# Kernel optimization log

Hardware: AMD Instinct MI355X
Metric: run time of the kernel (lower is better)

Reference implementation:

```python
import jax, jax.numpy as jnp
import numpy as np

# NF4 codebook (bitsandbytes nf4 data type, 16 levels)
NF4_TABLE = np.array([
    -1.0, -0.6961928009986877, -0.5250730514526367, -0.39491748809814453,
    -0.28444138169288635, -0.18477343022823334, -0.09105003625154495, 0.0,
    0.07958029955625534, 0.16093020141124725, 0.24611230194568634,
    0.33791524171829224, 0.44070982933044434, 0.5626170039176941,
    0.7229568362236023, 1.0], dtype=np.float32)

BLOCKSIZE = 64
SCALING = 32.0 / 16.0  # lora_alpha / r


def setup_inputs() -> dict:
    key = jax.random.key(0)
    k1, k2, k3, k4, k5 = jax.random.split(key, 5)
    tokens, in_f, out_f, r = 256, 4096, 11008, 16
    x = jax.random.normal(k1, (tokens, in_f), dtype=jnp.float32)
    q_codes = jax.random.randint(k2, (out_f, in_f), 0, 16, dtype=jnp.int32)
    absmax = jax.random.uniform(k3, (out_f, in_f // BLOCKSIZE), dtype=jnp.float32)
    lora_A = jax.random.normal(k4, (r, in_f), dtype=jnp.float32) * (1.0 / np.sqrt(in_f))
    lora_B = jax.random.normal(k5, (out_f, r), dtype=jnp.float32) * 0.02
    return {"x": x, "q_codes": q_codes, "absmax": absmax,
            "lora_A": lora_A, "lora_B": lora_B}


def reference(x, q_codes, absmax, lora_A, lora_B):
    out_f, in_f = q_codes.shape
    nf4 = jnp.asarray(NF4_TABLE, dtype=x.dtype)
    # Dequantize: codebook lookup, then per-block absmax scale.
    W = nf4[q_codes].reshape(out_f, in_f // BLOCKSIZE, BLOCKSIZE)
    W = (W * absmax[:, :, None]).reshape(out_f, in_f)  # [out_f, in_f]
    # Base 4-bit linear (no bias in bnb Linear4bit default here).
    base = x @ W.T  # [tokens, out_f]
    # LoRA path: dropout p=0 is identity in eval; scaling = alpha/r.
    lora = (x @ lora_A.T) @ lora_B.T  # [tokens, r] -> [tokens, out_f]
    return base + lora * jnp.asarray(SCALING, dtype=x.dtype)
```

## Files before the change

### kernel.cpp

```cpp
#include <hip/hip_runtime.h>
#include <hip/hip_fp16.h>

typedef unsigned int uint;
typedef unsigned short ushort;

typedef __attribute__((ext_vector_type(8))) _Float16 f16x8;
typedef __attribute__((ext_vector_type(4))) float f32x4;

#define TOK 256
#define OUTF 11008
#define INF 4096
#define BM 256
#define BN 64
#define NT2 172

__device__ __constant__ float NF4_TBL[16] = {
    -1.0f, -0.6961928009986877f, -0.5250730514526367f, -0.39491748809814453f,
    -0.28444138169288635f, -0.18477343022823334f, -0.09105003625154495f, 0.0f,
    0.07958029955625534f, 0.16093020141124725f, 0.24611230194568634f,
    0.33791524171829224f, 0.44070982933044434f, 0.5626170039176941f,
    0.7229568362236023f, 1.0f};

__device__ __forceinline__ ushort f2h(float f) {
  return __half_as_ushort(__float2half(f));
}

__device__ __forceinline__ void async_cp16(const void* g, void* l) {
  __builtin_amdgcn_global_load_lds(
      (const __attribute__((address_space(1))) uint*)g,
      (__attribute__((address_space(3))) uint*)l, 16, 0, 0);
}

__global__ void prep_kernel(const int4* __restrict__ qc4, uint* __restrict__ pk,
                            const float4* __restrict__ x4, ushort4* __restrict__ xh4,
                            const float4* __restrict__ lB4, ushort4* __restrict__ lBh4) {
  const int stride = gridDim.x * blockDim.x;
  const int t0 = blockIdx.x * blockDim.x + threadIdx.x;
  for (int d = t0; d < OUTF * INF / 8; d += stride) {
    int4 a = qc4[2 * d];
    int4 b = qc4[2 * d + 1];
    pk[d] = (uint)(a.x & 15) | ((uint)(a.y & 15) << 4) | ((uint)(a.z & 15) << 8) |
            ((uint)(a.w & 15) << 12) | ((uint)(b.x & 15) << 16) | ((uint)(b.y & 15) << 20) |
            ((uint)(b.z & 15) << 24) | ((uint)(b.w & 15) << 28);
  }
  for (int i = t0; i < TOK * INF / 4; i += stride) {
    float4 v = x4[i];
    ushort4 o;
    o.x = f2h(v.x); o.y = f2h(v.y); o.z = f2h(v.z); o.w = f2h(v.w);
    xh4[i] = o;
  }
  for (int i = t0; i < OUTF * 16; i += stride) {
    int n = i >> 4, jq = i & 15;
    ushort4 o = {0, 0, 0, 0};
    if (jq < 4) {
      float4 v = lB4[n * 4 + jq];
      o.x = f2h(v.x); o.y = f2h(v.y); o.z = f2h(v.z); o.w = f2h(v.w);
    }
    lBh4[i] = o;
  }
}

__global__ __launch_bounds__(1024)
void xa_kernel(const float* __restrict__ x, const float* __restrict__ lA,
               ushort* __restrict__ xa2) {
  const int m = blockIdx.x;
  const int t = threadIdx.x;
  const float4* x4 = (const float4*)(x + (size_t)m * INF);
  const float4* lA4 = (const float4*)lA;
  float4 xv = x4[t];
  float acc[16];
#pragma unroll
  for (int j = 0; j < 16; ++j) {
    float4 a = lA4[j * (INF / 4) + t];
    acc[j] = xv.x * a.x + xv.y * a.y + xv.z * a.z + xv.w * a.w;
  }
#pragma unroll
  for (int j = 0; j < 16; ++j)
#pragma unroll
    for (int s = 32; s > 0; s >>= 1) acc[j] += __shfl_xor(acc[j], s, 64);
  __shared__ float red[16][16];
  const int w = t >> 6, l = t & 63;
  if (l == 0) {
#pragma unroll
    for (int j = 0; j < 16; ++j) red[w][j] = acc[j];
  }
  __syncthreads();
  if (t < 64) {
    ushort v = 0;
    if (t < 16) {
      float s = 0.f;
#pragma unroll
      for (int w2 = 0; w2 < 16; ++w2) s += red[w2][t];
      v = f2h(2.0f * s);
    }
    xa2[m * 64 + t] = v;
  }
}

__global__ __launch_bounds__(256, 3)
void gemm_kernel(const uint* __restrict__ pk, const float* __restrict__ am,
                 const ushort* __restrict__ xh, const ushort* __restrict__ lBh,
                 const ushort* __restrict__ xa2, float* __restrict__ dest, int nst) {
  __shared__ ushort Abuf[BM * 64];
  __shared__ __half2 tbl[256];

  const int tid = threadIdx.x;
  const int w = tid >> 6;
  const int l = tid & 63;
  const int chunk = l >> 4;
  const int rlo = l & 15;
  const int split = blockIdx.x / NT2;
  const int ntile = blockIdx.x - split * NT2;
  const int n0 = ntile * BN;
  const int k0 = split * nst * 64;

  tbl[tid & 255] = __halves2half2(__float2half(NF4_TBL[tid & 15]),
                                  __float2half(NF4_TBL[(tid >> 4) & 15]));

  const int arow = w * 8 + (l >> 3);
  const int acol = ((l & 7) ^ (l >> 3)) << 3;

  int aoff[2][4];
#pragma unroll
  for (int ks2 = 0; ks2 < 2; ++ks2) {
    const int cc = ks2 * 4 + chunk;
#pragma unroll
    for (int mt = 0; mt < 4; ++mt)
      aoff[ks2][mt] = (w * 64 + mt * 16 + rlo) * 64 + ((cc ^ (l & 7)) << 3);
  }

  int col[4];
  const char* qp[4];
  const float* amp[4];
#pragma unroll
  for (int nt = 0; nt < 4; ++nt) {
    col[nt] = n0 + nt * 16 + rlo;
    qp[nt] = (const char*)pk + (size_t)col[nt] * (INF / 2) + (k0 >> 1) + chunk * 4;
    amp[nt] = am + (size_t)col[nt] * 64 + (k0 >> 6);
  }

  f32x4 acc[4][4];
#pragma unroll
  for (int mt = 0; mt < 4; ++mt)
#pragma unroll
    for (int nt = 0; nt < 4; ++nt) acc[mt][nt] = (f32x4){0.f, 0.f, 0.f, 0.f};

#pragma unroll
  for (int i = 0; i < 8; ++i) {
    const ushort* g = xh + (size_t)(i * 32 + arow) * INF + k0 + acol;
    async_cp16(g, &Abuf[(i * 256 + w * 64) * 8]);
  }
  uint qd[2][8];
  float ax[2][4];
#pragma unroll
  for (int nt = 0; nt < 4; ++nt) {
    qd[0][nt * 2 + 0] = *(const uint*)(qp[nt]);
    qd[0][nt * 2 + 1] = *(const uint*)(qp[nt] + 16);
    ax[0][nt] = amp[nt][0];
  }

#pragma unroll 2
  for (int s = 0; s < nst; ++s) {
    const int p = s & 1;
    __syncthreads();

    f16x8 areg[2][4];
#pragma unroll
    for (int ks2 = 0; ks2 < 2; ++ks2)
#pragma unroll
      for (int mt = 0; mt < 4; ++mt) areg[ks2][mt] = *(const f16x8*)&Abuf[aoff[ks2][mt]];

    __syncthreads();

    if (s + 1 < nst) {
      const int kb = k0 + (s + 1) * 64;
#pragma unroll
      for (int i = 0; i < 8; ++i) {
        const ushort* g = xh + (size_t)(i * 32 + arow) * INF + kb + acol;
        async_cp16(g, &Abuf[(i * 256 + w * 64) * 8]);
      }
    }
    const int sq = (s + 1 < nst) ? (s + 1) : (nst - 1);
#pragma unroll
    for (int nt = 0; nt < 4; ++nt) {
      qd[p ^ 1][nt * 2 + 0] = *(const uint*)(qp[nt] + sq * 32);
      qd[p ^ 1][nt * 2 + 1] = *(const uint*)(qp[nt] + sq * 32 + 16);
      ax[p ^ 1][nt] = amp[nt][sq];
    }

#pragma unroll
    for (int ks2 = 0; ks2 < 2; ++ks2) {
      f16x8 b[4];
#pragma unroll
      for (int nt = 0; nt < 4; ++nt) {
        uint dw = qd[p][nt * 2 + ks2];
        __half2 ax2 = __float2half2_rn(ax[p][nt]);
        union { __half2 h[4]; f16x8 v; } u;
        u.h[0] = __hmul2(tbl[dw & 255], ax2);
        u.h[1] = __hmul2(tbl[(dw >> 8) & 255], ax2);
        u.h[2] = __hmul2(tbl[(dw >> 16) & 255], ax2);
        u.h[3] = __hmul2(tbl[dw >> 24], ax2);
        b[nt] = u.v;
      }
#pragma unroll
      for (int mt = 0; mt < 4; ++mt)
#pragma unroll
        for (int nt = 0; nt < 4; ++nt)
          acc[mt][nt] = __builtin_amdgcn_mfma_f32_16x16x32_f16(areg[ks2][mt], b[nt], acc[mt][nt], 0, 0, 0);
    }
  }

  if (split == 0) {
    f16x8 a_l[4], b_l[4];
#pragma unroll
    for (int mt = 0; mt < 4; ++mt)
      a_l[mt] = *(const f16x8*)(xa2 + (size_t)(w * 64 + mt * 16 + rlo) * 64 + chunk * 8);
#pragma unroll
    for (int nt = 0; nt < 4; ++nt)
      b_l[nt] = *(const f16x8*)(lBh + (size_t)col[nt] * 64 + chunk * 8);
#pragma unroll
    for (int mt = 0; mt < 4; ++mt)
#pragma unroll
      for (int nt = 0; nt < 4; ++nt)
        acc[mt][nt] = __builtin_amdgcn_mfma_f32_16x16x32_f16(a_l[mt], b_l[nt], acc[mt][nt], 0, 0, 0);
  }

  float* dst = dest + (size_t)split * TOK * OUTF;
#pragma unroll
  for (int mt = 0; mt < 4; ++mt) {
#pragma unroll
    for (int nt = 0; nt < 4; ++nt) {
      int c = col[nt];
#pragma unroll
      for (int r = 0; r < 4; ++r) {
        int row = w * 64 + mt * 16 + chunk * 4 + r;
        dst[(size_t)row * OUTF + c] = acc[mt][nt][r];
      }
    }
  }
}

__global__ void reduce_kernel(const float4* __restrict__ part, float4* __restrict__ out,
                              int ks) {
  const int QN = TOK * OUTF / 4;
  int i = blockIdx.x * blockDim.x + threadIdx.x;
  if (i < QN) {
    float4 s = part[i];
    for (int s2 = 1; s2 < ks; ++s2) {
      float4 p = part[(size_t)s2 * QN + i];
      s.x += p.x; s.y += p.y; s.z += p.z; s.w += p.w;
    }
    out[i] = s;
  }
}

extern "C" void kernel_launch(void* const* d_in, const int* in_sizes, int n_in,
                              void* d_out, int out_size, void* d_ws, size_t ws_size,
                              hipStream_t stream) {
  const float* x = (const float*)d_in[0];
  const int* qc = (const int*)d_in[1];
  const float* am = (const float*)d_in[2];
  const float* lA = (const float*)d_in[3];
  const float* lB = (const float*)d_in[4];
  float* out = (float*)d_out;

  const size_t off_lB = (size_t)TOK * INF * 2;
  const size_t off_xa2 = off_lB + (size_t)OUTF * 64 * 2;
  const size_t off_pk = off_xa2 + (size_t)TOK * 64 * 2;
  const size_t off_part = off_pk + (size_t)OUTF * INF / 2;
  const size_t part_bytes = (size_t)TOK * OUTF * 4;

  ushort* xh = (ushort*)d_ws;
  ushort* lBh = (ushort*)((char*)d_ws + off_lB);
  ushort* xa2 = (ushort*)((char*)d_ws + off_xa2);
  uint* pk = (uint*)((char*)d_ws + off_pk);
  float* part = (float*)((char*)d_ws + off_part);

  int ks = 1;
  if (ws_size >= off_part + 8 * part_bytes) ks = 8;
  else if (ws_size >= off_part + 4 * part_bytes) ks = 4;
  else if (ws_size >= off_part + 2 * part_bytes) ks = 2;
  float* dest = (ks == 1) ? out : part;

  prep_kernel<<<4096, 256, 0, stream>>>((const int4*)qc, pk, (const float4*)x,
                                        (ushort4*)xh, (const float4*)lB, (ushort4*)lBh);
  xa_kernel<<<TOK, 1024, 0, stream>>>(x, lA, xa2);
  gemm_kernel<<<NT2 * ks, 256, 0, stream>>>(pk, am, xh, lBh, xa2, dest, 64 / ks);
  if (ks > 1)
    reduce_kernel<<<(TOK * OUTF / 4 + 255) / 256, 256, 0, stream>>>((const float4*)part,
                                                                    (float4*)out, ks);
}
```

Baseline: 386.5 us.

## Dequantize NF4 tile once per block into shared memory instead of per wave

Previously all four waves dequantized the same 64-column weight tile into registers, repeating identical lookup and scale work four times. Now packed codes and absmax values are staged into LDS with async copies. Each wave dequantizes a quarter of the tile into a swizzled shared B buffer, and all waves read MFMA operands from it. The maximum split-K factor also drops from 8 to 4, which cuts partial-sum traffic and reduction work but leaves fewer blocks. The cost is extra LDS use, which may lower occupancy, and a dependency of dequantization on the per-step barriers.

Measured after the change: 314.1 us. 18.7% less time.

```diff
diff --git a/kernel.cpp b/kernel.cpp
--- a/kernel.cpp
+++ b/kernel.cpp
@@ -102,6 +102,9 @@
                  const ushort* __restrict__ xh, const ushort* __restrict__ lBh,
                  const ushort* __restrict__ xa2, float* __restrict__ dest, int nst) {
   __shared__ ushort Abuf[BM * 64];
+  __shared__ ushort Bbuf[64 * 64];
+  __shared__ uint Qbuf[512];
+  __shared__ float Qax[1024];
   __shared__ __half2 tbl[256];
 
   const int tid = threadIdx.x;
@@ -112,14 +115,13 @@
   const int split = blockIdx.x / NT2;
   const int ntile = blockIdx.x - split * NT2;
   const int n0 = ntile * BN;
-  const int k0 = split * nst * 64;
+  const int kb0 = split * nst;
 
   tbl[tid & 255] = __halves2half2(__float2half(NF4_TBL[tid & 15]),
                                   __float2half(NF4_TBL[(tid >> 4) & 15]));
 
   const int arow = w * 8 + (l >> 3);
   const int acol = ((l & 7) ^ (l >> 3)) << 3;
-
   int aoff[2][4];
 #pragma unroll
   for (int ks2 = 0; ks2 < 2; ++ks2) {
@@ -129,15 +131,17 @@
       aoff[ks2][mt] = (w * 64 + mt * 16 + rlo) * 64 + ((cc ^ (l & 7)) << 3);
   }
 
-  int col[4];
-  const char* qp[4];
-  const float* amp[4];
-#pragma unroll
-  for (int nt = 0; nt < 4; ++nt) {
-    col[nt] = n0 + nt * 16 + rlo;
-    qp[nt] = (const char*)pk + (size_t)col[nt] * (INF / 2) + (k0 >> 1) + chunk * 4;
-    amp[nt] = am + (size_t)col[nt] * 64 + (k0 >> 6);
-  }
+  const int dr = tid & 63;
+  const int p7 = dr & 7;
+  const int bw0 = dr * 64 + ((w ^ p7) << 3);
+  const int bw1 = dr * 64 + (((w + 4) ^ p7) << 3);
+
+  int boff[2][4];
+#pragma unroll
+  for (int ks2 = 0; ks2 < 2; ++ks2)
+#pragma unroll
+    for (int nt = 0; nt < 4; ++nt)
+      boff[ks2][nt] = (nt * 16 + rlo) * 64 + (((ks2 * 4 + chunk) ^ (rlo & 7)) << 3);
 
   f32x4 acc[4][4];
 #pragma unroll
@@ -145,25 +149,44 @@
 #pragma unroll
     for (int nt = 0; nt < 4; ++nt) acc[mt][nt] = (f32x4){0.f, 0.f, 0.f, 0.f};
 
+  if (w == 0) {
+#pragma unroll
+    for (int j = 0; j < 4; ++j)
+      async_cp16(am + (size_t)(n0 + l) * 64 + kb0 + j * 4, (char*)Qax + j * 1024);
+#pragma unroll
+    for (int j = 0; j < 2; ++j)
+      async_cp16((const char*)pk + (size_t)(n0 + l) * 2048 + kb0 * 32 + j * 16,
+                 (char*)Qbuf + j * 1024);
+  }
 #pragma unroll
   for (int i = 0; i < 8; ++i) {
-    const ushort* g = xh + (size_t)(i * 32 + arow) * INF + k0 + acol;
+    const ushort* g = xh + (size_t)(i * 32 + arow) * INF + kb0 * 64 + acol;
     async_cp16(g, &Abuf[(i * 256 + w * 64) * 8]);
   }
-  uint qd[2][8];
-  float ax[2][4];
-#pragma unroll
-  for (int nt = 0; nt < 4; ++nt) {
-    qd[0][nt * 2 + 0] = *(const uint*)(qp[nt]);
-    qd[0][nt * 2 + 1] = *(const uint*)(qp[nt] + 16);
-    ax[0][nt] = amp[nt][0];
-  }
-
-#pragma unroll 2
+
   for (int s = 0; s < nst; ++s) {
-    const int p = s & 1;
     __syncthreads();
 
+    uint q0 = Qbuf[dr * 4 + w];
+    uint q1 = Qbuf[256 + dr * 4 + w];
+    const int sl = s & 15;
+    __half2 ax2 = __float2half2_rn(Qax[(sl >> 2) * 256 + dr * 4 + (sl & 3)]);
+    {
+      union { __half2 h[4]; f16x8 v; } u;
+      u.h[0] = __hmul2(tbl[q0 & 255], ax2);
+      u.h[1] = __hmul2(tbl[(q0 >> 8) & 255], ax2);
+      u.h[2] = __hmul2(tbl[(q0 >> 16) & 255], ax2);
+      u.h[3] = __hmul2(tbl[q0 >> 24], ax2);
+      *(f16x8*)&Bbuf[bw0] = u.v;
+    }
+    {
+      union { __half2 h[4]; f16x8 v; } u;
+      u.h[0] = __hmul2(tbl[q1 & 255], ax2);
+      u.h[1] = __hmul2(tbl[(q1 >> 8) & 255], ax2);
+      u.h[2] = __hmul2(tbl[(q1 >> 16) & 255], ax2);
+      u.h[3] = __hmul2(tbl[q1 >> 24], ax2);
+      *(f16x8*)&Bbuf[bw1] = u.v;
+    }
     f16x8 areg[2][4];
 #pragma unroll
     for (int ks2 = 0; ks2 < 2; ++ks2)
@@ -173,35 +196,30 @@
     __syncthreads();
 
     if (s + 1 < nst) {
-      const int kb = k0 + (s + 1) * 64;
+      const int kb = kb0 + s + 1;
 #pragma unroll
       for (int i = 0; i < 8; ++i) {
-        const ushort* g = xh + (size_t)(i * 32 + arow) * INF + kb + acol;
+        const ushort* g = xh + (size_t)(i * 32 + arow) * INF + kb * 64 + acol;
         async_cp16(g, &Abuf[(i * 256 + w * 64) * 8]);
       }
-    }
-    const int sq = (s + 1 < nst) ? (s + 1) : (nst - 1);
-#pragma unroll
-    for (int nt = 0; nt < 4; ++nt) {
-      qd[p ^ 1][nt * 2 + 0] = *(const uint*)(qp[nt] + sq * 32);
-      qd[p ^ 1][nt * 2 + 1] = *(const uint*)(qp[nt] + sq * 32 + 16);
-      ax[p ^ 1][nt] = amp[nt][sq];
+      if (w == 0) {
+#pragma unroll
+        for (int j = 0; j < 2; ++j)
+          async_cp16((const char*)pk + (size_t)(n0 + l) * 2048 + kb * 32 + j * 16,
+                     (char*)Qbuf + j * 1024);
+        if (((s + 1) & 15) == 0) {
+#pragma unroll
+          for (int j = 0; j < 4; ++j)
+            async_cp16(am + (size_t)(n0 + l) * 64 + kb + j * 4, (char*)Qax + j * 1024);
+        }
+      }
     }
 
 #pragma unroll
     for (int ks2 = 0; ks2 < 2; ++ks2) {
       f16x8 b[4];
 #pragma unroll
-      for (int nt = 0; nt < 4; ++nt) {
-        uint dw = qd[p][nt * 2 + ks2];
-        __half2 ax2 = __float2half2_rn(ax[p][nt]);
-        union { __half2 h[4]; f16x8 v; } u;
-        u.h[0] = __hmul2(tbl[dw & 255], ax2);
-        u.h[1] = __hmul2(tbl[(dw >> 8) & 255], ax2);
-        u.h[2] = __hmul2(tbl[(dw >> 16) & 255], ax2);
-        u.h[3] = __hmul2(tbl[dw >> 24], ax2);
-        b[nt] = u.v;
-      }
+      for (int nt = 0; nt < 4; ++nt) b[nt] = *(const f16x8*)&Bbuf[boff[ks2][nt]];
 #pragma unroll
       for (int mt = 0; mt < 4; ++mt)
 #pragma unroll
@@ -217,7 +235,7 @@
       a_l[mt] = *(const f16x8*)(xa2 + (size_t)(w * 64 + mt * 16 + rlo) * 64 + chunk * 8);
 #pragma unroll
     for (int nt = 0; nt < 4; ++nt)
-      b_l[nt] = *(const f16x8*)(lBh + (size_t)col[nt] * 64 + chunk * 8);
+      b_l[nt] = *(const f16x8*)(lBh + (size_t)(n0 + nt * 16 + rlo) * 64 + chunk * 8);
 #pragma unroll
     for (int mt = 0; mt < 4; ++mt)
 #pragma unroll
@@ -230,7 +248,7 @@
   for (int mt = 0; mt < 4; ++mt) {
 #pragma unroll
     for (int nt = 0; nt < 4; ++nt) {
-      int c = col[nt];
+      int c = n0 + nt * 16 + rlo;
 #pragma unroll
       for (int r = 0; r < 4; ++r) {
         int row = w * 64 + mt * 16 + chunk * 4 + r;
@@ -277,8 +295,7 @@
   float* part = (float*)((char*)d_ws + off_part);
 
   int ks = 1;
-  if (ws_size >= off_part + 8 * part_bytes) ks = 8;
-  else if (ws_size >= off_part + 4 * part_bytes) ks = 4;
+  if (ws_size >= off_part + 4 * part_bytes) ks = 4;
   else if (ws_size >= off_part + 2 * part_bytes) ks = 2;
   float* dest = (ks == 1) ? out : part;
 
```
